# Kernel optimization log

Measured on AMD Instinct MI355X. Metric: run time of the kernel, lower is better.

Reference implementation:

```python
import jax, jax.numpy as jnp
import numpy as np

FIELD_DIMS = [1000000, 100000, 1008, 1004, 102, 1000, 500, 50, 112, 107]
B = 16384
EMB = 32
DENSE = 16
MLP = [256, 128, 64]
BN_EPS = 1e-5
V_TOTAL = int(np.sum(FIELD_DIMS))
OFFSETS = jnp.asarray(np.concatenate([[0], np.cumsum(FIELD_DIMS)[:-1]]), dtype=jnp.int64)


def _xavier(key, fan_out, fan_in):
    lim = float(np.sqrt(6.0 / (fan_in + fan_out)))
    return jax.random.uniform(key, (fan_out, fan_in), jnp.float32, -lim, lim)


def setup_inputs() -> dict:
    key = jax.random.key(0)
    ks = jax.random.split(key, 16)
    # per-field in-range indices, stacked to [B, n_fields]
    sparse_cols = [jax.random.randint(jax.random.fold_in(ks[0], i), (B,), 0, d)
                   for i, d in enumerate(FIELD_DIMS)]
    sparse_inputs = jnp.stack(sparse_cols, axis=1).astype(jnp.int64)
    dense_inputs = jax.random.normal(ks[1], (B, DENSE), jnp.float32)
    # concatenated embedding / first-order bias tables (same math as per-field nn.Embedding)
    emb_table = 0.01 * jax.random.normal(ks[2], (V_TOTAL, EMB), jnp.float32)
    bias_table = 0.01 * jax.random.normal(ks[3], (V_TOTAL, 1), jnp.float32)
    fm_bias = jnp.zeros((1,), jnp.float32)
    dims = [len(FIELD_DIMS) * EMB + DENSE] + MLP
    params = {}
    for li in range(len(MLP)):
        params[f"W{li}"] = _xavier(ks[4 + li], dims[li + 1], dims[li])
        params[f"b{li}"] = jnp.zeros((dims[li + 1],), jnp.float32)
        params[f"g{li}"] = jnp.ones((dims[li + 1],), jnp.float32)
        params[f"be{li}"] = jnp.zeros((dims[li + 1],), jnp.float32)
    Wo = _xavier(ks[10], 1, MLP[-1])
    bo = jnp.zeros((1,), jnp.float32)
    return dict(sparse_inputs=sparse_inputs, dense_inputs=dense_inputs,
                emb_table=emb_table, bias_table=bias_table, fm_bias=fm_bias,
                Wo=Wo, bo=bo, **params)


def reference(sparse_inputs, dense_inputs, emb_table, bias_table, fm_bias,
              Wo, bo, W0, b0, g0, be0, W1, b1, g1, be1, W2, b2, g2, be2):
    idx = sparse_inputs + OFFSETS[None, :]           # [B, F] global rows
    field_embs = emb_table[idx]                      # [B, F, E] multi-table gather
    # FM first order: sum of per-field scalar biases
    fm_first = bias_table[idx][..., 0].sum(axis=1)   # [B]
    # FM second order: 0.5 * sum_d ((sum_f e)^2 - sum_f e^2)
    s = field_embs.sum(axis=1)                       # [B, E]
    sq = (field_embs * field_embs).sum(axis=1)       # [B, E]
    fm_second = 0.5 * (s * s - sq).sum(axis=-1)      # [B]
    fm_out = fm_bias[0] + fm_first + fm_second
    # deep component (BatchNorm in eval mode at init stats: mean=0, var=1; dropout=identity)
    x = jnp.concatenate([field_embs.reshape(field_embs.shape[0], -1), dense_inputs], axis=-1)
    inv = 1.0 / jnp.sqrt(1.0 + BN_EPS)
    for W, b, g, be in ((W0, b0, g0, be0), (W1, b1, g1, be1), (W2, b2, g2, be2)):
        h = x @ W.T + b
        h = h * (g * inv) + be
        x = jax.nn.relu(h)
    deep_out = (x @ Wo.T + bo)[:, 0]
    return jax.nn.sigmoid(fm_out + deep_out)
```

## Files before the change

kernel.cpp:

```cpp
#include <hip/hip_runtime.h>
#include <hip/hip_bf16.h>
#include <math.h>

#define BROWS 16384
#define NF    10
#define EMB   32
#define DENSE 16
#define K0S   352
#define K0    336
#define N0    256
#define N1    128
#define N2    64
#define BN_INV 0.99999500003749969f

__constant__ int c_offsets[NF] = {
    0, 1000000, 1100000, 1101008, 1102012,
    1102114, 1103114, 1103614, 1103664, 1103776
};

typedef short  bf16x8 __attribute__((ext_vector_type(8)));
typedef float  f32x4  __attribute__((ext_vector_type(4)));

static __device__ __forceinline__ unsigned short f2bf(float x) {
    union { float f; unsigned u; } c; c.f = x;
    unsigned r = (c.u + 0x7FFFu + ((c.u >> 16) & 1u)) >> 16;
    return (unsigned short)r;
}

__global__ __launch_bounds__(256) void k_wconv_all(
    const float* __restrict__ W0, const float* __restrict__ W1,
    const float* __restrict__ W2,
    unsigned short* __restrict__ W0b, unsigned short* __restrict__ W1b,
    unsigned short* __restrict__ W2b)
{
    int i = blockIdx.x * 256 + threadIdx.x;
    if (i < N0 * K0S) {
        int r = i / K0S, c = i - r * K0S;
        W0b[i] = f2bf(c < K0 ? W0[r * K0 + c] : 0.f);
    } else if (i < N0 * K0S + N1 * N0) {
        int j = i - N0 * K0S;
        W1b[j] = f2bf(W1[j]);
    } else {
        int j = i - (N0 * K0S + N1 * N0);
        W2b[j] = f2bf(W2[j]);
    }
}

__global__ __launch_bounds__(256) void k_fused_all(
    const int*   __restrict__ sparse,
    const float* __restrict__ dense,
    const float* __restrict__ emb,
    const float* __restrict__ bias_tab,
    const float* __restrict__ fm_bias,
    const unsigned short* __restrict__ W0b,
    const float* __restrict__ b0, const float* __restrict__ g0,
    const float* __restrict__ be0,
    const unsigned short* __restrict__ W1b,
    const float* __restrict__ b1, const float* __restrict__ g1,
    const float* __restrict__ be1,
    const unsigned short* __restrict__ W2b,
    const float* __restrict__ b2, const float* __restrict__ g2,
    const float* __restrict__ be2,
    const float* __restrict__ Wo,
    const float* __restrict__ bo,
    float* __restrict__ out)
{
    __shared__ unsigned short x1s[32][N0 + 2];
    __shared__ unsigned short h2s[32][N1 + 2];
    __shared__ float fmld[32];
    __shared__ float partial[2][32];

    const int tid  = threadIdx.x;
    const int wave = tid >> 6;
    const int lane = tid & 63;
    const int l16  = lane & 15;
    const int quad = lane >> 4;
    const int rg   = wave & 1;
    const int hh   = wave >> 1;
    const int bm   = blockIdx.x * 32;
    const int arow = bm + rg * 16 + l16;

    int idx[NF];
#pragma unroll
    for (int f = 0; f < NF; ++f)
        idx[f] = sparse[arow * NF + f] + c_offsets[f];

    float first = 0.f, sq = 0.f;
    float s8[8];
#pragma unroll
    for (int j = 0; j < 8; ++j) s8[j] = 0.f;

    if (hh == 0 && quad == 0) {
#pragma unroll
        for (int f = 0; f < NF; ++f) first += bias_tab[idx[f]];
    }

    f32x4 acc1[8];
#pragma unroll
    for (int nt = 0; nt < 8; ++nt) acc1[nt] = (f32x4){0.f, 0.f, 0.f, 0.f};

    const unsigned short* wp0 = W0b + (size_t)(hh * 128 + l16) * K0S + quad * 8;

#pragma unroll
    for (int f = 0; f < NF; ++f) {
        const float4* ep = (const float4*)(emb + (size_t)idx[f] * EMB) + quad * 2;
        float4 v0 = ep[0];
        float4 v1 = ep[1];
        if (hh == 0) {
            s8[0] += v0.x; s8[1] += v0.y; s8[2] += v0.z; s8[3] += v0.w;
            s8[4] += v1.x; s8[5] += v1.y; s8[6] += v1.z; s8[7] += v1.w;
            sq += v0.x*v0.x + v0.y*v0.y + v0.z*v0.z + v0.w*v0.w
                + v1.x*v1.x + v1.y*v1.y + v1.z*v1.z + v1.w*v1.w;
        }
        bf16x8 a;
        a[0] = (short)f2bf(v0.x); a[1] = (short)f2bf(v0.y);
        a[2] = (short)f2bf(v0.z); a[3] = (short)f2bf(v0.w);
        a[4] = (short)f2bf(v1.x); a[5] = (short)f2bf(v1.y);
        a[6] = (short)f2bf(v1.z); a[7] = (short)f2bf(v1.w);
#pragma unroll
        for (int nt = 0; nt < 8; ++nt) {
            bf16x8 w = *(const bf16x8*)(wp0 + (size_t)(nt * 16) * K0S + f * 32);
            acc1[nt] = __builtin_amdgcn_mfma_f32_16x16x32_bf16(a, w, acc1[nt], 0, 0, 0);
        }
    }
    {
        bf16x8 a;
        if (quad < 2) {
            const float4* dp = (const float4*)(dense + arow * DENSE) + quad * 2;
            float4 v0 = dp[0];
            float4 v1 = dp[1];
            a[0] = (short)f2bf(v0.x); a[1] = (short)f2bf(v0.y);
            a[2] = (short)f2bf(v0.z); a[3] = (short)f2bf(v0.w);
            a[4] = (short)f2bf(v1.x); a[5] = (short)f2bf(v1.y);
            a[6] = (short)f2bf(v1.z); a[7] = (short)f2bf(v1.w);
        } else {
#pragma unroll
            for (int j = 0; j < 8; ++j) a[j] = 0;
        }
#pragma unroll
        for (int nt = 0; nt < 8; ++nt) {
            bf16x8 w = *(const bf16x8*)(wp0 + (size_t)(nt * 16) * K0S + 320);
            acc1[nt] = __builtin_amdgcn_mfma_f32_16x16x32_bf16(a, w, acc1[nt], 0, 0, 0);
        }
    }

    if (hh == 0) {
        float ss = 0.f;
#pragma unroll
        for (int j = 0; j < 8; ++j) ss += s8[j] * s8[j];
        ss += __shfl_xor(ss, 16); ss += __shfl_xor(ss, 32);
        sq += __shfl_xor(sq, 16); sq += __shfl_xor(sq, 32);
        first += __shfl_xor(first, 16); first += __shfl_xor(first, 32);
        if (quad == 0)
            fmld[rg * 16 + l16] = fm_bias[0] + first + 0.5f * (ss - sq);
    }

#pragma unroll
    for (int nt = 0; nt < 8; ++nt) {
        int col = hh * 128 + nt * 16 + l16;
        float sc = g0[col] * BN_INV;
        float tb = fmaf(b0[col], sc, be0[col]);
#pragma unroll
        for (int r = 0; r < 4; ++r) {
            float v = fmaf(acc1[nt][r], sc, tb);
            v = v > 0.f ? v : 0.f;
            x1s[rg * 16 + quad * 4 + r][col] = f2bf(v);
        }
    }
    __syncthreads();

    f32x4 acc2[4];
#pragma unroll
    for (int nt = 0; nt < 4; ++nt) acc2[nt] = (f32x4){0.f, 0.f, 0.f, 0.f};
    const unsigned short* wp1 = W1b + (size_t)(hh * 64 + l16) * N0 + quad * 8;
#pragma unroll
    for (int ks = 0; ks < 8; ++ks) {
        bf16x8 a = *(const bf16x8*)(&x1s[rg * 16 + l16][ks * 32 + quad * 8]);
#pragma unroll
        for (int nt = 0; nt < 4; ++nt) {
            bf16x8 w = *(const bf16x8*)(wp1 + (size_t)(nt * 16) * N0 + ks * 32);
            acc2[nt] = __builtin_amdgcn_mfma_f32_16x16x32_bf16(a, w, acc2[nt], 0, 0, 0);
        }
    }
#pragma unroll
    for (int nt = 0; nt < 4; ++nt) {
        int col = hh * 64 + nt * 16 + l16;
        float sc = g1[col] * BN_INV;
        float tb = fmaf(b1[col], sc, be1[col]);
#pragma unroll
        for (int r = 0; r < 4; ++r) {
            float v = fmaf(acc2[nt][r], sc, tb);
            v = v > 0.f ? v : 0.f;
            h2s[rg * 16 + quad * 4 + r][col] = f2bf(v);
        }
    }
    __syncthreads();

    f32x4 acc3[2];
#pragma unroll
    for (int nt = 0; nt < 2; ++nt) acc3[nt] = (f32x4){0.f, 0.f, 0.f, 0.f};
    const unsigned short* wp2 = W2b + (size_t)(hh * 32 + l16) * N1 + quad * 8;
#pragma unroll
    for (int ks = 0; ks < 4; ++ks) {
        bf16x8 a = *(const bf16x8*)(&h2s[rg * 16 + l16][ks * 32 + quad * 8]);
#pragma unroll
        for (int nt = 0; nt < 2; ++nt) {
            bf16x8 w = *(const bf16x8*)(wp2 + (size_t)(nt * 16) * N1 + ks * 32);
            acc3[nt] = __builtin_amdgcn_mfma_f32_16x16x32_bf16(a, w, acc3[nt], 0, 0, 0);
        }
    }

    float p[4] = {0.f, 0.f, 0.f, 0.f};
#pragma unroll
    for (int nt = 0; nt < 2; ++nt) {
        int col = hh * 32 + nt * 16 + l16;
        float sc = g2[col] * BN_INV;
        float tb = fmaf(b2[col], sc, be2[col]);
        float wo = Wo[col];
#pragma unroll
        for (int r = 0; r < 4; ++r) {
            float v = fmaf(acc3[nt][r], sc, tb);
            v = v > 0.f ? v : 0.f;
            p[r] = fmaf(v, wo, p[r]);
        }
    }
#pragma unroll
    for (int r = 0; r < 4; ++r) {
        p[r] += __shfl_xor(p[r], 1);
        p[r] += __shfl_xor(p[r], 2);
        p[r] += __shfl_xor(p[r], 4);
        p[r] += __shfl_xor(p[r], 8);
    }
    if (l16 == 0) {
#pragma unroll
        for (int r = 0; r < 4; ++r)
            partial[hh][rg * 16 + quad * 4 + r] = p[r];
    }
    __syncthreads();

    if (tid < 32) {
        float z = fmld[tid] + partial[0][tid] + partial[1][tid] + bo[0];
        out[bm + tid] = 1.f / (1.f + expf(-z));
    }
}

extern "C" void kernel_launch(void* const* d_in, const int* in_sizes, int n_in,
                              void* d_out, int out_size, void* d_ws, size_t ws_size,
                              hipStream_t stream)
{
    const int*   sparse   = (const int*)  d_in[0];
    const float* dense    = (const float*)d_in[1];
    const float* emb      = (const float*)d_in[2];
    const float* bias_tab = (const float*)d_in[3];
    const float* fm_bias  = (const float*)d_in[4];
    const float* Wo       = (const float*)d_in[5];
    const float* bo       = (const float*)d_in[6];
    const float* W0 = (const float*)d_in[7];
    const float* b0 = (const float*)d_in[8];
    const float* g0 = (const float*)d_in[9];
    const float* be0= (const float*)d_in[10];
    const float* W1 = (const float*)d_in[11];
    const float* b1 = (const float*)d_in[12];
    const float* g1 = (const float*)d_in[13];
    const float* be1= (const float*)d_in[14];
    const float* W2 = (const float*)d_in[15];
    const float* b2 = (const float*)d_in[16];
    const float* g2 = (const float*)d_in[17];
    const float* be2= (const float*)d_in[18];

    float* out = (float*)d_out;

    char* p = (char*)d_ws;
    unsigned short* W0b = (unsigned short*)p; p += (size_t)N0 * K0S * 2;
    unsigned short* W1b = (unsigned short*)p; p += (size_t)N1 * N0 * 2;
    unsigned short* W2b = (unsigned short*)p; p += (size_t)N2 * N1 * 2;

    k_wconv_all<<<(N0 * K0S + N1 * N0 + N2 * N1) / 256, 256, 0, stream>>>(
        W0, W1, W2, W0b, W1b, W2b);

    k_fused_all<<<BROWS / 32, 256, 0, stream>>>(
        sparse, dense, emb, bias_tab, fm_bias,
        W0b, b0, g0, be0, W1b, b1, g1, be1, W2b, b2, g2, be2,
        Wo, bo, out);
}
```

Measured before the change: 235.7 us.

## Split work so each block handles 16 rows with four waves across columns

Each block now covers 16 batch rows instead of 32, and its four waves split the output columns of every layer four ways instead of using a 2x2 row/column split. This doubles the grid to 1024 blocks and halves per-wave accumulator registers, aiming at better occupancy and latency hiding for the embedding gathers. In exchange, each weight tile is reloaded for half as many rows, and only one of four waves computes the FM terms. The bf16 packing also switches to the paired __float22bfloat162_rn conversion to cut per-element conversion instructions.

```diff
diff --git a/kernel.cpp b/kernel.cpp
--- a/kernel.cpp
+++ b/kernel.cpp
@@ -21,10 +21,16 @@
 typedef short  bf16x8 __attribute__((ext_vector_type(8)));
 typedef float  f32x4  __attribute__((ext_vector_type(4)));
 
+union Frag { bf16x8 v; unsigned u[4]; };
+
 static __device__ __forceinline__ unsigned short f2bf(float x) {
     union { float f; unsigned u; } c; c.f = x;
     unsigned r = (c.u + 0x7FFFu + ((c.u >> 16) & 1u)) >> 16;
     return (unsigned short)r;
+}
+static __device__ __forceinline__ unsigned pk2(float x, float y) {
+    __hip_bfloat162 h = __float22bfloat162_rn(make_float2(x, y));
+    union { __hip_bfloat162 h; unsigned u; } c; c.h = h; return c.u;
 }
 
 __global__ __launch_bounds__(256) void k_wconv_all(
@@ -65,20 +71,18 @@
     const float* __restrict__ bo,
     float* __restrict__ out)
 {
-    __shared__ unsigned short x1s[32][N0 + 2];
-    __shared__ unsigned short h2s[32][N1 + 2];
-    __shared__ float fmld[32];
-    __shared__ float partial[2][32];
+    __shared__ unsigned short x1s[16][N0 + 2];
+    __shared__ unsigned short h2s[16][N1 + 2];
+    __shared__ float fmld[16];
+    __shared__ float partial[4][16];
 
     const int tid  = threadIdx.x;
-    const int wave = tid >> 6;
+    const int wq   = tid >> 6;
     const int lane = tid & 63;
     const int l16  = lane & 15;
     const int quad = lane >> 4;
-    const int rg   = wave & 1;
-    const int hh   = wave >> 1;
-    const int bm   = blockIdx.x * 32;
-    const int arow = bm + rg * 16 + l16;
+    const int bm   = blockIdx.x * 16;
+    const int arow = bm + l16;
 
     int idx[NF];
 #pragma unroll
@@ -90,61 +94,56 @@
 #pragma unroll
     for (int j = 0; j < 8; ++j) s8[j] = 0.f;
 
-    if (hh == 0 && quad == 0) {
+    if (wq == 0 && quad == 0) {
 #pragma unroll
         for (int f = 0; f < NF; ++f) first += bias_tab[idx[f]];
     }
 
-    f32x4 acc1[8];
-#pragma unroll
-    for (int nt = 0; nt < 8; ++nt) acc1[nt] = (f32x4){0.f, 0.f, 0.f, 0.f};
-
-    const unsigned short* wp0 = W0b + (size_t)(hh * 128 + l16) * K0S + quad * 8;
+    f32x4 acc1[4];
+#pragma unroll
+    for (int nt = 0; nt < 4; ++nt) acc1[nt] = (f32x4){0.f, 0.f, 0.f, 0.f};
+
+    const unsigned short* wp0 = W0b + (size_t)(wq * 64 + l16) * K0S + quad * 8;
 
 #pragma unroll
     for (int f = 0; f < NF; ++f) {
         const float4* ep = (const float4*)(emb + (size_t)idx[f] * EMB) + quad * 2;
         float4 v0 = ep[0];
         float4 v1 = ep[1];
-        if (hh == 0) {
+        if (wq == 0) {
             s8[0] += v0.x; s8[1] += v0.y; s8[2] += v0.z; s8[3] += v0.w;
             s8[4] += v1.x; s8[5] += v1.y; s8[6] += v1.z; s8[7] += v1.w;
             sq += v0.x*v0.x + v0.y*v0.y + v0.z*v0.z + v0.w*v0.w
                 + v1.x*v1.x + v1.y*v1.y + v1.z*v1.z + v1.w*v1.w;
         }
-        bf16x8 a;
-        a[0] = (short)f2bf(v0.x); a[1] = (short)f2bf(v0.y);
-        a[2] = (short)f2bf(v0.z); a[3] = (short)f2bf(v0.w);
-        a[4] = (short)f2bf(v1.x); a[5] = (short)f2bf(v1.y);
-        a[6] = (short)f2bf(v1.z); a[7] = (short)f2bf(v1.w);
-#pragma unroll
-        for (int nt = 0; nt < 8; ++nt) {
+        Frag a;
+        a.u[0] = pk2(v0.x, v0.y); a.u[1] = pk2(v0.z, v0.w);
+        a.u[2] = pk2(v1.x, v1.y); a.u[3] = pk2(v1.z, v1.w);
+#pragma unroll
+        for (int nt = 0; nt < 4; ++nt) {
             bf16x8 w = *(const bf16x8*)(wp0 + (size_t)(nt * 16) * K0S + f * 32);
-            acc1[nt] = __builtin_amdgcn_mfma_f32_16x16x32_bf16(a, w, acc1[nt], 0, 0, 0);
+            acc1[nt] = __builtin_amdgcn_mfma_f32_16x16x32_bf16(a.v, w, acc1[nt], 0, 0, 0);
         }
     }
     {
-        bf16x8 a;
+        Frag a;
         if (quad < 2) {
             const float4* dp = (const float4*)(dense + arow * DENSE) + quad * 2;
             float4 v0 = dp[0];
             float4 v1 = dp[1];
-            a[0] = (short)f2bf(v0.x); a[1] = (short)f2bf(v0.y);
-            a[2] = (short)f2bf(v0.z); a[3] = (short)f2bf(v0.w);
-            a[4] = (short)f2bf(v1.x); a[5] = (short)f2bf(v1.y);
-            a[6] = (short)f2bf(v1.z); a[7] = (short)f2bf(v1.w);
+            a.u[0] = pk2(v0.x, v0.y); a.u[1] = pk2(v0.z, v0.w);
+            a.u[2] = pk2(v1.x, v1.y); a.u[3] = pk2(v1.z, v1.w);
         } else {
-#pragma unroll
-            for (int j = 0; j < 8; ++j) a[j] = 0;
-        }
-#pragma unroll
-        for (int nt = 0; nt < 8; ++nt) {
+            a.u[0] = 0; a.u[1] = 0; a.u[2] = 0; a.u[3] = 0;
+        }
+#pragma unroll
+        for (int nt = 0; nt < 4; ++nt) {
             bf16x8 w = *(const bf16x8*)(wp0 + (size_t)(nt * 16) * K0S + 320);
-            acc1[nt] = __builtin_amdgcn_mfma_f32_16x16x32_bf16(a, w, acc1[nt], 0, 0, 0);
-        }
-    }
-
-    if (hh == 0) {
+            acc1[nt] = __builtin_amdgcn_mfma_f32_16x16x32_bf16(a.v, w, acc1[nt], 0, 0, 0);
+        }
+    }
+
+    if (wq == 0) {
         float ss = 0.f;
 #pragma unroll
         for (int j = 0; j < 8; ++j) ss += s8[j] * s8[j];
@@ -152,76 +151,70 @@
         sq += __shfl_xor(sq, 16); sq += __shfl_xor(sq, 32);
         first += __shfl_xor(first, 16); first += __shfl_xor(first, 32);
         if (quad == 0)
-            fmld[rg * 16 + l16] = fm_bias[0] + first + 0.5f * (ss - sq);
-    }
-
-#pragma unroll
-    for (int nt = 0; nt < 8; ++nt) {
-        int col = hh * 128 + nt * 16 + l16;
+            fmld[l16] = fm_bias[0] + first + 0.5f * (ss - sq);
+    }
+
+#pragma unroll
+    for (int nt = 0; nt < 4; ++nt) {
+        int col = wq * 64 + nt * 16 + l16;
         float sc = g0[col] * BN_INV;
         float tb = fmaf(b0[col], sc, be0[col]);
 #pragma unroll
         for (int r = 0; r < 4; ++r) {
             float v = fmaf(acc1[nt][r], sc, tb);
             v = v > 0.f ? v : 0.f;
-            x1s[rg * 16 + quad * 4 + r][col] = f2bf(v);
+            x1s[quad * 4 + r][col] = f2bf(v);
         }
     }
     __syncthreads();
 
-    f32x4 acc2[4];
-#pragma unroll
-    for (int nt = 0; nt < 4; ++nt) acc2[nt] = (f32x4){0.f, 0.f, 0.f, 0.f};
-    const unsigned short* wp1 = W1b + (size_t)(hh * 64 + l16) * N0 + quad * 8;
+    f32x4 acc2[2];
+#pragma unroll
+    for (int nt = 0; nt < 2; ++nt) acc2[nt] = (f32x4){0.f, 0.f, 0.f, 0.f};
+    const unsigned short* wp1 = W1b + (size_t)(wq * 32 + l16) * N0 + quad * 8;
 #pragma unroll
     for (int ks = 0; ks < 8; ++ks) {
-        bf16x8 a = *(const bf16x8*)(&x1s[rg * 16 + l16][ks * 32 + quad * 8]);
-#pragma unroll
-        for (int nt = 0; nt < 4; ++nt) {
+        bf16x8 a = *(const bf16x8*)(&x1s[l16][ks * 32 + quad * 8]);
+#pragma unroll
+        for (int nt = 0; nt < 2; ++nt) {
             bf16x8 w = *(const bf16x8*)(wp1 + (size_t)(nt * 16) * N0 + ks * 32);
             acc2[nt] = __builtin_amdgcn_mfma_f32_16x16x32_bf16(a, w, acc2[nt], 0, 0, 0);
         }
     }
 #pragma unroll
-    for (int nt = 0; nt < 4; ++nt) {
-        int col = hh * 64 + nt * 16 + l16;
+    for (int nt = 0; nt < 2; ++nt) {
+        int col = wq * 32 + nt * 16 + l16;
         float sc = g1[col] * BN_INV;
         float tb = fmaf(b1[col], sc, be1[col]);
 #pragma unroll
         for (int r = 0; r < 4; ++r) {
             float v = fmaf(acc2[nt][r], sc, tb);
             v = v > 0.f ? v : 0.f;
-            h2s[rg * 16 + quad * 4 + r][col] = f2bf(v);
+            h2s[quad * 4 + r][col] = f2bf(v);
         }
     }
     __syncthreads();
 
-    f32x4 acc3[2];
-#pragma unroll
-    for (int nt = 0; nt < 2; ++nt) acc3[nt] = (f32x4){0.f, 0.f, 0.f, 0.f};
-    const unsigned short* wp2 = W2b + (size_t)(hh * 32 + l16) * N1 + quad * 8;
+    f32x4 acc3 = (f32x4){0.f, 0.f, 0.f, 0.f};
+    const unsigned short* wp2 = W2b + (size_t)(wq * 16 + l16) * N1 + quad * 8;
 #pragma unroll
     for (int ks = 0; ks < 4; ++ks) {
-        bf16x8 a = *(const bf16x8*)(&h2s[rg * 16 + l16][ks * 32 + quad * 8]);
-#pragma unroll
-        for (int nt = 0; nt < 2; ++nt) {
-            bf16x8 w = *(const bf16x8*)(wp2 + (size_t)(nt * 16) * N1 + ks * 32);
-            acc3[nt] = __builtin_amdgcn_mfma_f32_16x16x32_bf16(a, w, acc3[nt], 0, 0, 0);
-        }
-    }
-
-    float p[4] = {0.f, 0.f, 0.f, 0.f};
-#pragma unroll
-    for (int nt = 0; nt < 2; ++nt) {
-        int col = hh * 32 + nt * 16 + l16;
+        bf16x8 a = *(const bf16x8*)(&h2s[l16][ks * 32 + quad * 8]);
+        bf16x8 w = *(const bf16x8*)(wp2 + ks * 32);
+        acc3 = __builtin_amdgcn_mfma_f32_16x16x32_bf16(a, w, acc3, 0, 0, 0);
+    }
+
+    float p[4];
+    {
+        int col = wq * 16 + l16;
         float sc = g2[col] * BN_INV;
         float tb = fmaf(b2[col], sc, be2[col]);
         float wo = Wo[col];
 #pragma unroll
         for (int r = 0; r < 4; ++r) {
-            float v = fmaf(acc3[nt][r], sc, tb);
+            float v = fmaf(acc3[r], sc, tb);
             v = v > 0.f ? v : 0.f;
-            p[r] = fmaf(v, wo, p[r]);
+            p[r] = v * wo;
         }
     }
 #pragma unroll
@@ -234,12 +227,13 @@
     if (l16 == 0) {
 #pragma unroll
         for (int r = 0; r < 4; ++r)
-            partial[hh][rg * 16 + quad * 4 + r] = p[r];
+            partial[wq][quad * 4 + r] = p[r];
     }
     __syncthreads();
 
-    if (tid < 32) {
-        float z = fmld[tid] + partial[0][tid] + partial[1][tid] + bo[0];
+    if (tid < 16) {
+        float z = fmld[tid] + partial[0][tid] + partial[1][tid]
+                + partial[2][tid] + partial[3][tid] + bo[0];
         out[bm + tid] = 1.f / (1.f + expf(-z));
     }
 }
@@ -278,7 +272,7 @@
     k_wconv_all<<<(N0 * K0S + N1 * N0 + N2 * N1) / 256, 256, 0, stream>>>(
         W0, W1, W2, W0b, W1b, W2b);
 
-    k_fused_all<<<BROWS / 32, 256, 0, stream>>>(
+    k_fused_all<<<BROWS / 16, 256, 0, stream>>>(
         sparse, dense, emb, bias_tab, fm_bias,
         W0b, b0, g0, be0, W1b, b1, g1, be1, W2b, b2, g2, be2,
         Wo, bo, out);
```

After: 241.9 us. +2.6%, slower.
